# Kernel optimization log

Measured on AMD Instinct MI355X. Metric: run time of the kernel, lower is better.

The kernel has to match this reference:

```python
import jax, jax.numpy as jnp
import numpy as np

B, S, HID = 2, 2048, 2048
NH, NKV, HD = 32, 8, 64
ROPE_THETA = 10000.0
SCALE = HD ** -0.5


def _rope_cos_sin(seq_len, head_dim, theta):
    inv_freq = 1.0 / (theta ** (jnp.arange(0, head_dim, 2, dtype=jnp.float32) / head_dim))
    pos = jnp.arange(seq_len, dtype=jnp.float32)
    freqs = jnp.outer(pos, inv_freq)              # [S, HD/2]
    emb = jnp.concatenate([freqs, freqs], axis=-1)  # [S, HD]
    return jnp.cos(emb), jnp.sin(emb)


def _rotate_half(x):
    x1, x2 = jnp.split(x, 2, axis=-1)
    return jnp.concatenate([-x2, x1], axis=-1)


def setup_inputs() -> dict:
    key = jax.random.key(0)
    ks = jax.random.split(key, 8)
    s = 0.02
    return {
        "hidden_states": jax.random.normal(ks[0], (B, S, HID), jnp.float32),
        "q_w": jax.random.normal(ks[1], (NH * HD, HID), jnp.float32) * s,
        "q_b": jax.random.normal(ks[2], (NH * HD,), jnp.float32) * s,
        "k_w": jax.random.normal(ks[3], (NKV * HD, HID), jnp.float32) * s,
        "k_b": jax.random.normal(ks[4], (NKV * HD,), jnp.float32) * s,
        "v_w": jax.random.normal(ks[5], (NKV * HD, HID), jnp.float32) * s,
        "v_b": jax.random.normal(ks[6], (NKV * HD,), jnp.float32) * s,
        "o_w": jax.random.normal(ks[7], (HID, NH * HD), jnp.float32) * s,
    }


def reference(hidden_states, q_w, q_b, k_w, k_b, v_w, v_b, o_w):
    bsz, q_len, _ = hidden_states.shape
    # QKV projections (nn.Linear: x @ W^T + b)
    q = hidden_states @ q_w.T + q_b   # [B, S, NH*HD]
    k = hidden_states @ k_w.T + k_b   # [B, S, NKV*HD]
    v = hidden_states @ v_w.T + v_b
    # reshape to [B, H, S, D]
    q = q.reshape(bsz, q_len, NH, HD).transpose(0, 2, 1, 3)
    k = k.reshape(bsz, q_len, NKV, HD).transpose(0, 2, 1, 3)
    v = v.reshape(bsz, q_len, NKV, HD).transpose(0, 2, 1, 3)
    # RoPE
    cos, sin = _rope_cos_sin(q_len, HD, ROPE_THETA)  # [S, HD]
    cos = cos[None, None]; sin = sin[None, None]
    q = q * cos + _rotate_half(q) * sin
    k = k * cos + _rotate_half(k) * sin
    # GQA: expand kv heads to match query heads
    groups = NH // NKV
    k = jnp.repeat(k, groups, axis=1)  # [B, NH, S, D]
    v = jnp.repeat(v, groups, axis=1)
    # scaled dot-product attention with causal mask
    scores = jnp.einsum('bhqd,bhkd->bhqk', q, k) * SCALE
    causal = jnp.tril(jnp.ones((q_len, q_len), dtype=bool))
    scores = jnp.where(causal[None, None], scores, jnp.finfo(scores.dtype).min)
    probs = jax.nn.softmax(scores, axis=-1)
    out = jnp.einsum('bhqk,bhkd->bhqd', probs, v)  # [B, NH, S, D]
    out = out.transpose(0, 2, 1, 3).reshape(bsz, q_len, NH * HD)
    return out @ o_w.T  # [B, S, HID]
```

## Files before the change

kernel.cpp:

```cpp
#include <hip/hip_runtime.h>
#include <stdint.h>
#include <stddef.h>

typedef __attribute__((ext_vector_type(8))) short s16x8;
typedef __attribute__((ext_vector_type(4))) short s16x4;
typedef __attribute__((ext_vector_type(4))) float f32x4;
typedef __attribute__((ext_vector_type(2))) unsigned int u32x2;

#define S_LEN 2048
#define HID 2048
#define QKV_N 3072
#define NHEAD 32
#define NKVH 8

__device__ __forceinline__ unsigned short f2bf(float f) {
  union { float f; unsigned u; } a; a.f = f;
  unsigned u = a.u;
  u += 0x7fffu + ((u >> 16) & 1u);
  return (unsigned short)(u >> 16);
}
__device__ __forceinline__ unsigned cvt_pk_bf16(float a, float b) {
  unsigned r;
  asm("v_cvt_pk_bf16_f32 %0, %1, %2" : "=v"(r) : "v"(a), "v"(b));
  return r;
}
__device__ __forceinline__ void gl_lds16(const unsigned short* g, short* l) {
  __builtin_amdgcn_global_load_lds(
      (const __attribute__((address_space(1))) unsigned int*)g,
      (__attribute__((address_space(3))) unsigned int*)l, 16, 0, 0);
}

__global__ void k_convert(const float* __restrict__ x, const float* __restrict__ wq,
                          const float* __restrict__ wk, const float* __restrict__ wv,
                          const float* __restrict__ wo, unsigned short* __restrict__ dst) {
  const unsigned n4 = 18874368u / 4u;
  for (unsigned i = blockIdx.x * blockDim.x + threadIdx.x; i < n4;
       i += gridDim.x * blockDim.x) {
    unsigned e = i * 4u;
    const float* src; unsigned off;
    if (e < 8388608u)       { src = x;  off = e; }
    else if (e < 12582912u) { src = wq; off = e - 8388608u; }
    else if (e < 13631488u) { src = wk; off = e - 12582912u; }
    else if (e < 14680064u) { src = wv; off = e - 13631488u; }
    else                    { src = wo; off = e - 14680064u; }
    f32x4 v = *(const f32x4*)(src + off);
    s16x4 o;
    o[0] = (short)f2bf(v[0]); o[1] = (short)f2bf(v[1]);
    o[2] = (short)f2bf(v[2]); o[3] = (short)f2bf(v[3]);
    *(s16x4*)(dst + e) = o;
  }
}

__global__ void k_rope_table(float* __restrict__ cost, float* __restrict__ sint) {
  int idx = blockIdx.x * 256 + threadIdx.x;
  int i = idx & 31, s = idx >> 5;
  float inv = powf(10000.0f, -(float)(2 * i) / 64.0f);
  float ang = (float)s * inv;
  cost[idx] = cosf(ang);
  sint[idx] = sinf(ang);
}

template <int MODE>
__global__ __launch_bounds__(256) void k_gemm(
    const unsigned short* __restrict__ A,
    const unsigned short* __restrict__ W0, const unsigned short* __restrict__ W1,
    const unsigned short* __restrict__ W2,
    const float* __restrict__ b0, const float* __restrict__ b1, const float* __restrict__ b2,
    const float* __restrict__ ct, const float* __restrict__ st,
    unsigned short* __restrict__ Cb, float* __restrict__ Cf) {
  __shared__ short lA[3][4096];
  __shared__ short lB[3][4096];
  const int K = 2048;
  int tid = threadIdx.x;
  int wave = tid >> 6, lane = tid & 63;
  int l15 = lane & 15, lg = lane >> 4;
  int nwg = gridDim.x * gridDim.y;
  int f = blockIdx.y * gridDim.x + blockIdx.x;
  f = (f & 7) * (nwg >> 3) + (f >> 3);
  int tn = f % gridDim.x, tm = f / gridDim.x;

  const unsigned short* W; const float* bias = nullptr; int col0;
  if constexpr (MODE == 0) {
    if (tn < 16)      { W = W0; bias = b0; col0 = tn * 128; }
    else if (tn < 20) { W = W1; bias = b1; col0 = (tn - 16) * 128; }
    else              { W = W2; bias = b2; col0 = (tn - 20) * 128; }
  } else { W = W0; col0 = tn * 128; }
  int m0 = tm * 128;
  int wm = wave >> 1, wn = wave & 1;

  const unsigned short* gA0 = A + (size_t)(m0 + (tid >> 2)) * K + (tid & 3) * 8;
  const unsigned short* gA1 = gA0 + (size_t)64 * K;
  const unsigned short* gB0 = W + (size_t)(col0 + (tid >> 2)) * K + (tid & 3) * 8;
  const unsigned short* gB1 = gB0 + (size_t)64 * K;

  f32x4 acc[4][4];
#pragma unroll
  for (int m = 0; m < 4; ++m)
#pragma unroll
    for (int n = 0; n < 4; ++n) acc[m][n] = (f32x4){0.f, 0.f, 0.f, 0.f};

#pragma unroll
  for (int p = 0; p < 2; ++p) {
    int off = p * 32;
    gl_lds16(gA0 + off, &lA[p][wave * 512]);
    gl_lds16(gA1 + off, &lA[p][2048 + wave * 512]);
    gl_lds16(gB0 + off, &lB[p][wave * 512]);
    gl_lds16(gB1 + off, &lB[p][2048 + wave * 512]);
  }

  int cur = 0;
  for (int kt = 0; kt < 64; ++kt) {
    asm volatile("s_waitcnt vmcnt(4)" ::: "memory");
    __builtin_amdgcn_s_barrier();
    __builtin_amdgcn_sched_barrier(0);
    if (kt + 2 < 64) {
      int nx = cur + 2; if (nx >= 3) nx -= 3;
      int off = (kt + 2) * 32;
      gl_lds16(gA0 + off, &lA[nx][wave * 512]);
      gl_lds16(gA1 + off, &lA[nx][2048 + wave * 512]);
      gl_lds16(gB0 + off, &lB[nx][wave * 512]);
      gl_lds16(gB1 + off, &lB[nx][2048 + wave * 512]);
    }
    s16x8 af[4], bfr[4];
    const short* pa = &lA[cur][(wm * 64 + l15) * 32 + lg * 8];
    const short* pb = &lB[cur][(wn * 64 + l15) * 32 + lg * 8];
#pragma unroll
    for (int m = 0; m < 4; ++m) af[m] = *(const s16x8*)(pa + m * 512);
#pragma unroll
    for (int n = 0; n < 4; ++n) bfr[n] = *(const s16x8*)(pb + n * 512);
    __builtin_amdgcn_s_setprio(1);
#pragma unroll
    for (int m = 0; m < 4; ++m)
#pragma unroll
      for (int n = 0; n < 4; ++n)
        acc[m][n] = __builtin_amdgcn_mfma_f32_16x16x32_bf16(af[m], bfr[n], acc[m][n], 0, 0, 0);
    __builtin_amdgcn_s_setprio(0);
    cur = (cur + 1 == 3) ? 0 : cur + 1;
  }

  if constexpr (MODE == 0) {
    const float CSC = 0.125f * 1.44269504f;
    bool rope = (tn < 20);
    bool isq = (tn < 16);
#pragma unroll
    for (int n = 0; n < 2; ++n) {
      int lcol = col0 + wn * 64 + n * 16 + l15;
      int gcol = tn * 128 + wn * 64 + n * 16 + l15;
      float blo = bias[lcol], bhi = bias[lcol + 32];
      int i = n * 16 + l15;
#pragma unroll
      for (int m = 0; m < 4; ++m) {
        int row = m0 + wm * 64 + m * 16 + lg * 4;
#pragma unroll
        for (int r = 0; r < 4; ++r) {
          float xl = acc[m][n][r] + blo;
          float xh = acc[m][n + 2][r] + bhi;
          if (rope) {
            int s = (row + r) & (S_LEN - 1);
            float c = ct[s * 32 + i], sn = st[s * 32 + i];
            float nl = xl * c - xh * sn;
            xh = xh * c + xl * sn;
            xl = nl;
            if (isq) { xl *= CSC; xh *= CSC; }
          }
          Cb[(size_t)(row + r) * QKV_N + gcol] = f2bf(xl);
          Cb[(size_t)(row + r) * QKV_N + gcol + 32] = f2bf(xh);
        }
      }
    }
  } else {
#pragma unroll
    for (int n = 0; n < 4; ++n) {
      int gcol = tn * 128 + wn * 64 + n * 16 + l15;
#pragma unroll
      for (int m = 0; m < 4; ++m) {
        int row = m0 + wm * 64 + m * 16 + lg * 4;
#pragma unroll
        for (int r = 0; r < 4; ++r)
          Cf[(size_t)(row + r) * HID + gcol] = acc[m][n][r];
      }
    }
  }
}

__global__ void k_vtrans(const unsigned short* __restrict__ qkv, unsigned short* __restrict__ vt) {
  __shared__ unsigned short t[64][80];
  int ts = blockIdx.x & 63, td = blockIdx.x >> 6;
  int tid = threadIdx.x;
#pragma unroll
  for (int L = 0; L < 2; ++L) {
    int c = L * 256 + tid;
    int row = c >> 3, ch = c & 7;
    const unsigned short* src = qkv + (size_t)(ts * 64 + row) * QKV_N + 2560 + td * 64 + ch * 8;
    s16x8 v = *(const s16x8*)src;
    int cs = (ch * 8) ^ ((row >> 3) << 3);
    *(s16x8*)&t[row][cs] = v;
  }
  __syncthreads();
  int b = (ts * 64) >> 11;
  int s0 = (ts * 64) & (S_LEN - 1);
#pragma unroll
  for (int L = 0; L < 2; ++L) {
    int c = L * 256 + tid;
    int d = c >> 3, sc = c & 7;
    s16x8 o;
#pragma unroll
    for (int j = 0; j < 8; ++j) o[j] = (short)t[sc * 8 + j][d ^ (sc << 3)];
    unsigned short* dst = vt + ((size_t)((b * 8 + td) * 64 + d)) * 2048 + s0 + sc * 8;
    *(s16x8*)dst = o;
  }
}

__global__ __launch_bounds__(512, 4) void k_attn(const unsigned short* __restrict__ qkv,
                                                 const unsigned short* __restrict__ vt,
                                                 unsigned short* __restrict__ aout) {
  __shared__ unsigned short lK[2][4096];
  __shared__ unsigned short lV[2][4096];
  __shared__ unsigned short pl[8][1024];
  int wave = threadIdx.x >> 6, lane = threadIdx.x & 63;
  int l15 = lane & 15, lg = lane >> 4;
  int bi = blockIdx.x;
  int t  = 63 - (bi >> 4);
  int b  = (bi >> 3) & 1;
  int hg = bi & 7;
  int wh = wave >> 1;
  int mh = wave & 1;
  int h  = hg * 4 + wh;
  int q0 = t * 32 + mh * 16;
  int kbmax = t >> 1;

  const unsigned short* qb_ = qkv + (size_t)(b * S_LEN) * QKV_N + h * 64;
  const unsigned short* kbase = qkv + (size_t)(b * S_LEN) * QKV_N + 2048 + hg * 64;
  const unsigned short* vbase = vt + (size_t)((b * NKVH + hg) * 64) * 2048;
  unsigned short* pw = &pl[wave][0];
  int sw = (l15 & 7) << 3;

  int srow = wave * 8 + (lane >> 3);
  int ssw = 8 * ((lane & 7) ^ ((lane >> 3) & 7));
  const unsigned short* gk0 = kbase + (size_t)srow * QKV_N + ssw;
  const unsigned short* gv0 = vbase + (size_t)srow * 2048 + ssw;
  short* lkd0 = (short*)&lK[0][wave * 512]; short* lkd1 = (short*)&lK[1][wave * 512];
  short* lvd0 = (short*)&lV[0][wave * 512]; short* lvd1 = (short*)&lV[1][wave * 512];

  s16x8 aq[2];
#pragma unroll
  for (int ks = 0; ks < 2; ++ks)
    aq[ks] = *(const s16x8*)(qb_ + (size_t)(q0 + l15) * QKV_N + ks * 32 + lg * 8);

  f32x4 acc[4];
#pragma unroll
  for (int dt = 0; dt < 4; ++dt) acc[dt] = (f32x4){0.f, 0.f, 0.f, 0.f};
  float lrow = 0.f;

  gl_lds16(gk0, lkd0);
  gl_lds16(gv0, lvd0);
  asm volatile("s_waitcnt vmcnt(0)" ::: "memory");
  __syncthreads();

  for (int kb = 0; kb <= kbmax; ++kb) {
    const unsigned short* lk = &lK[kb & 1][0];
    const unsigned short* lv = &lV[kb & 1][0];
    if (kb < kbmax) {
      size_t go = (size_t)(kb + 1) * 64;
      if ((kb & 1) == 0) { gl_lds16(gk0 + go * QKV_N, lkd1); gl_lds16(gv0 + go, lvd1); }
      else               { gl_lds16(gk0 + go * QKV_N, lkd0); gl_lds16(gv0 + go, lvd0); }
    }
    bool need_mask = (kb == kbmax);
    f32x4 z[4];
    __builtin_amdgcn_s_setprio(1);
#pragma unroll
    for (int nt = 0; nt < 4; ++nt) {
      s16x8 k0 = *(const s16x8*)(lk + (nt * 16 + l15) * 64 + ((lg * 8) ^ sw));
      s16x8 k1 = *(const s16x8*)(lk + (nt * 16 + l15) * 64 + ((32 + lg * 8) ^ sw));
      f32x4 zz = (f32x4){0.f, 0.f, 0.f, 0.f};
      zz = __builtin_amdgcn_mfma_f32_16x16x32_bf16(k0, aq[0], zz, 0, 0, 0);
      zz = __builtin_amdgcn_mfma_f32_16x16x32_bf16(k1, aq[1], zz, 0, 0, 0);
      z[nt] = zz;
    }
    __builtin_amdgcn_s_setprio(0);
    int q = q0 + l15;
    float rs = 0.f;
#pragma unroll
    for (int nt = 0; nt < 4; ++nt) {
      float p[4];
#pragma unroll
      for (int r = 0; r < 4; ++r) {
        float v = z[nt][r];
        if (need_mask) {
          int k = kb * 64 + nt * 16 + lg * 4 + r;
          if (k > q) v = -1.0e30f;
        }
        p[r] = __builtin_amdgcn_exp2f(v);
      }
      rs += (p[0] + p[1]) + (p[2] + p[3]);
      u32x2 w;
      w[0] = cvt_pk_bf16(p[0], p[1]);
      w[1] = cvt_pk_bf16(p[2], p[3]);
      *(u32x2*)(pw + l15 * 64 + ((nt * 16 + lg * 4) ^ sw)) = w;
    }
    rs += __shfl_xor(rs, 16);
    rs += __shfl_xor(rs, 32);
    lrow += rs;
    s16x8 pa0 = *(const s16x8*)(pw + l15 * 64 + ((lg * 8) ^ sw));
    s16x8 pa1 = *(const s16x8*)(pw + l15 * 64 + ((32 + lg * 8) ^ sw));
    __builtin_amdgcn_s_setprio(1);
#pragma unroll
    for (int dt = 0; dt < 4; ++dt) {
      s16x8 v0 = *(const s16x8*)(lv + (dt * 16 + l15) * 64 + ((lg * 8) ^ sw));
      s16x8 v1 = *(const s16x8*)(lv + (dt * 16 + l15) * 64 + ((32 + lg * 8) ^ sw));
      acc[dt] = __builtin_amdgcn_mfma_f32_16x16x32_bf16(pa0, v0, acc[dt], 0, 0, 0);
      acc[dt] = __builtin_amdgcn_mfma_f32_16x16x32_bf16(pa1, v1, acc[dt], 0, 0, 0);
    }
    __builtin_amdgcn_s_setprio(0);
    asm volatile("s_waitcnt vmcnt(0)" ::: "memory");
    __syncthreads();
  }

  unsigned short* ob = aout + (size_t)(b * S_LEN) * HID + h * 64;
#pragma unroll
  for (int r = 0; r < 4; ++r) {
    float lr = __shfl(lrow, lg * 4 + r);
    float inv = 1.0f / lr;
#pragma unroll
    for (int dt = 0; dt < 4; ++dt)
      ob[(size_t)(q0 + lg * 4 + r) * HID + dt * 16 + l15] = f2bf(acc[dt][r] * inv);
  }
}

extern "C" void kernel_launch(void* const* d_in, const int* in_sizes, int n_in,
                              void* d_out, int out_size, void* d_ws, size_t ws_size,
                              hipStream_t stream) {
  const float* x  = (const float*)d_in[0];
  const float* qw = (const float*)d_in[1];
  const float* qb = (const float*)d_in[2];
  const float* kw = (const float*)d_in[3];
  const float* kbias = (const float*)d_in[4];
  const float* vw = (const float*)d_in[5];
  const float* vbias = (const float*)d_in[6];
  const float* ow = (const float*)d_in[7];

  unsigned short* Xb  = (unsigned short*)d_ws;
  unsigned short* Wqb = Xb + 8388608;
  unsigned short* Wkb = Wqb + 4194304;
  unsigned short* Wvb = Wkb + 1048576;
  unsigned short* Wob = Wvb + 1048576;
  unsigned short* QKV = Wob + 4194304;
  unsigned short* VT  = QKV + 12582912;
  unsigned short* AO  = VT + 2097152;
  float* COS = (float*)(AO + 8388608);
  float* SIN = COS + 65536;

  k_convert<<<1024, 256, 0, stream>>>(x, qw, kw, vw, ow, Xb);
  k_rope_table<<<256, 256, 0, stream>>>(COS, SIN);
  k_gemm<0><<<dim3(24, 32), 256, 0, stream>>>(Xb, Wqb, Wkb, Wvb, qb, kbias, vbias,
                                              COS, SIN, QKV, nullptr);
  k_vtrans<<<512, 256, 0, stream>>>(QKV, VT);
  k_attn<<<1024, 512, 0, stream>>>(QKV, VT, AO);
  k_gemm<1><<<dim3(16, 32), 256, 0, stream>>>(AO, Wob, nullptr, nullptr,
                                              nullptr, nullptr, nullptr, nullptr, nullptr,
                                              nullptr, (float*)d_out);
}
```

Measured before the change: 190.9 us.

## Use dedicated 256x128 tile kernel with 8 waves for output projection GEMM

Splits the templated GEMM into a QKV kernel and a separate output-projection kernel that uses 512-thread blocks computing 256x128 tiles, so each B tile loaded into LDS is shared by twice as many rows. The output GEMM grid drops from 512 to 256 blocks, which halves redundant weight loads but leaves fewer blocks to fill the GPU. It also makes the last pipeline iteration wait for all outstanding loads (vmcnt(0)) instead of vmcnt(4), which tightens correctness of the triple-buffered prefetch.

```diff
diff --git a/kernel.cpp b/kernel.cpp
--- a/kernel.cpp
+++ b/kernel.cpp
@@ -60,14 +60,13 @@
   sint[idx] = sinf(ang);
 }
 
-template <int MODE>
-__global__ __launch_bounds__(256) void k_gemm(
+__global__ __launch_bounds__(256) void k_gemm0(
     const unsigned short* __restrict__ A,
     const unsigned short* __restrict__ W0, const unsigned short* __restrict__ W1,
     const unsigned short* __restrict__ W2,
     const float* __restrict__ b0, const float* __restrict__ b1, const float* __restrict__ b2,
     const float* __restrict__ ct, const float* __restrict__ st,
-    unsigned short* __restrict__ Cb, float* __restrict__ Cf) {
+    unsigned short* __restrict__ Cb) {
   __shared__ short lA[3][4096];
   __shared__ short lB[3][4096];
   const int K = 2048;
@@ -79,12 +78,10 @@
   f = (f & 7) * (nwg >> 3) + (f >> 3);
   int tn = f % gridDim.x, tm = f / gridDim.x;
 
-  const unsigned short* W; const float* bias = nullptr; int col0;
-  if constexpr (MODE == 0) {
-    if (tn < 16)      { W = W0; bias = b0; col0 = tn * 128; }
-    else if (tn < 20) { W = W1; bias = b1; col0 = (tn - 16) * 128; }
-    else              { W = W2; bias = b2; col0 = (tn - 20) * 128; }
-  } else { W = W0; col0 = tn * 128; }
+  const unsigned short* W; const float* bias; int col0;
+  if (tn < 16)      { W = W0; bias = b0; col0 = tn * 128; }
+  else if (tn < 20) { W = W1; bias = b1; col0 = (tn - 16) * 128; }
+  else              { W = W2; bias = b2; col0 = (tn - 20) * 128; }
   int m0 = tm * 128;
   int wm = wave >> 1, wn = wave & 1;
 
@@ -110,7 +107,8 @@
 
   int cur = 0;
   for (int kt = 0; kt < 64; ++kt) {
-    asm volatile("s_waitcnt vmcnt(4)" ::: "memory");
+    if (kt < 63) asm volatile("s_waitcnt vmcnt(4)" ::: "memory");
+    else         asm volatile("s_waitcnt vmcnt(0)" ::: "memory");
     __builtin_amdgcn_s_barrier();
     __builtin_amdgcn_sched_barrier(0);
     if (kt + 2 < 64) {
@@ -138,47 +136,112 @@
     cur = (cur + 1 == 3) ? 0 : cur + 1;
   }
 
-  if constexpr (MODE == 0) {
-    const float CSC = 0.125f * 1.44269504f;
-    bool rope = (tn < 20);
-    bool isq = (tn < 16);
-#pragma unroll
-    for (int n = 0; n < 2; ++n) {
-      int lcol = col0 + wn * 64 + n * 16 + l15;
-      int gcol = tn * 128 + wn * 64 + n * 16 + l15;
-      float blo = bias[lcol], bhi = bias[lcol + 32];
-      int i = n * 16 + l15;
-#pragma unroll
-      for (int m = 0; m < 4; ++m) {
-        int row = m0 + wm * 64 + m * 16 + lg * 4;
-#pragma unroll
-        for (int r = 0; r < 4; ++r) {
-          float xl = acc[m][n][r] + blo;
-          float xh = acc[m][n + 2][r] + bhi;
-          if (rope) {
-            int s = (row + r) & (S_LEN - 1);
-            float c = ct[s * 32 + i], sn = st[s * 32 + i];
-            float nl = xl * c - xh * sn;
-            xh = xh * c + xl * sn;
-            xl = nl;
-            if (isq) { xl *= CSC; xh *= CSC; }
-          }
-          Cb[(size_t)(row + r) * QKV_N + gcol] = f2bf(xl);
-          Cb[(size_t)(row + r) * QKV_N + gcol + 32] = f2bf(xh);
+  const float CSC = 0.125f * 1.44269504f;
+  bool rope = (tn < 20);
+  bool isq = (tn < 16);
+#pragma unroll
+  for (int n = 0; n < 2; ++n) {
+    int lcol = col0 + wn * 64 + n * 16 + l15;
+    int gcol = tn * 128 + wn * 64 + n * 16 + l15;
+    float blo = bias[lcol], bhi = bias[lcol + 32];
+    int i = n * 16 + l15;
+#pragma unroll
+    for (int m = 0; m < 4; ++m) {
+      int row = m0 + wm * 64 + m * 16 + lg * 4;
+#pragma unroll
+      for (int r = 0; r < 4; ++r) {
+        float xl = acc[m][n][r] + blo;
+        float xh = acc[m][n + 2][r] + bhi;
+        if (rope) {
+          int s = (row + r) & (S_LEN - 1);
+          float c = ct[s * 32 + i], sn = st[s * 32 + i];
+          float nl = xl * c - xh * sn;
+          xh = xh * c + xl * sn;
+          xl = nl;
+          if (isq) { xl *= CSC; xh *= CSC; }
         }
+        Cb[(size_t)(row + r) * QKV_N + gcol] = f2bf(xl);
+        Cb[(size_t)(row + r) * QKV_N + gcol + 32] = f2bf(xh);
       }
     }
-  } else {
-#pragma unroll
-    for (int n = 0; n < 4; ++n) {
-      int gcol = tn * 128 + wn * 64 + n * 16 + l15;
-#pragma unroll
-      for (int m = 0; m < 4; ++m) {
-        int row = m0 + wm * 64 + m * 16 + lg * 4;
-#pragma unroll
-        for (int r = 0; r < 4; ++r)
-          Cf[(size_t)(row + r) * HID + gcol] = acc[m][n][r];
-      }
+  }
+}
+
+__global__ __launch_bounds__(512, 4) void k_gemm2(
+    const unsigned short* __restrict__ A,
+    const unsigned short* __restrict__ W,
+    float* __restrict__ Cf) {
+  __shared__ short lA[3][8192];
+  __shared__ short lB[3][4096];
+  const int K = 2048;
+  int tid = threadIdx.x;
+  int wave = tid >> 6, lane = tid & 63;
+  int l15 = lane & 15, lg = lane >> 4;
+  int f = blockIdx.x;
+  f = (f & 7) * 32 + (f >> 3);
+  int tn = f & 15, tm = f >> 4;
+  int m0 = tm * 256, col0 = tn * 128;
+  int wm = wave >> 1, wn = wave & 1;
+
+  int sr = lane >> 2;
+  int sc = (lane & 3) * 8;
+  const unsigned short* gA0 = A + (size_t)(m0 + wave * 32 + sr) * K + sc;
+  const unsigned short* gA1 = gA0 + (size_t)16 * K;
+  const unsigned short* gB0 = W + (size_t)(col0 + wave * 16 + sr) * K + sc;
+
+  f32x4 acc[4][4];
+#pragma unroll
+  for (int m = 0; m < 4; ++m)
+#pragma unroll
+    for (int n = 0; n < 4; ++n) acc[m][n] = (f32x4){0.f, 0.f, 0.f, 0.f};
+
+#pragma unroll
+  for (int p = 0; p < 2; ++p) {
+    int off = p * 32;
+    gl_lds16(gA0 + off, &lA[p][wave * 1024 + lane * 8]);
+    gl_lds16(gA1 + off, &lA[p][wave * 1024 + 512 + lane * 8]);
+    gl_lds16(gB0 + off, &lB[p][wave * 512 + lane * 8]);
+  }
+
+  int cur = 0;
+  for (int kt = 0; kt < 64; ++kt) {
+    if (kt < 63) asm volatile("s_waitcnt vmcnt(3)" ::: "memory");
+    else         asm volatile("s_waitcnt vmcnt(0)" ::: "memory");
+    __builtin_amdgcn_s_barrier();
+    __builtin_amdgcn_sched_barrier(0);
+    if (kt + 2 < 64) {
+      int nx = cur + 2; if (nx >= 3) nx -= 3;
+      int off = (kt + 2) * 32;
+      gl_lds16(gA0 + off, &lA[nx][wave * 1024 + lane * 8]);
+      gl_lds16(gA1 + off, &lA[nx][wave * 1024 + 512 + lane * 8]);
+      gl_lds16(gB0 + off, &lB[nx][wave * 512 + lane * 8]);
+    }
+    s16x8 af[4], bfr[4];
+    const short* pa = &lA[cur][(wm * 64 + l15) * 32 + lg * 8];
+    const short* pb = &lB[cur][(wn * 64 + l15) * 32 + lg * 8];
+#pragma unroll
+    for (int m = 0; m < 4; ++m) af[m] = *(const s16x8*)(pa + m * 512);
+#pragma unroll
+    for (int n = 0; n < 4; ++n) bfr[n] = *(const s16x8*)(pb + n * 512);
+    __builtin_amdgcn_s_setprio(1);
+#pragma unroll
+    for (int m = 0; m < 4; ++m)
+#pragma unroll
+      for (int n = 0; n < 4; ++n)
+        acc[m][n] = __builtin_amdgcn_mfma_f32_16x16x32_bf16(af[m], bfr[n], acc[m][n], 0, 0, 0);
+    __builtin_amdgcn_s_setprio(0);
+    cur = (cur + 1 == 3) ? 0 : cur + 1;
+  }
+
+#pragma unroll
+  for (int n = 0; n < 4; ++n) {
+    int gcol = col0 + wn * 64 + n * 16 + l15;
+#pragma unroll
+    for (int m = 0; m < 4; ++m) {
+      int row = m0 + wm * 64 + m * 16 + lg * 4;
+#pragma unroll
+      for (int r = 0; r < 4; ++r)
+        Cf[(size_t)(row + r) * HID + gcol] = acc[m][n][r];
     }
   }
 }
@@ -352,11 +415,9 @@
 
   k_convert<<<1024, 256, 0, stream>>>(x, qw, kw, vw, ow, Xb);
   k_rope_table<<<256, 256, 0, stream>>>(COS, SIN);
-  k_gemm<0><<<dim3(24, 32), 256, 0, stream>>>(Xb, Wqb, Wkb, Wvb, qb, kbias, vbias,
-                                              COS, SIN, QKV, nullptr);
+  k_gemm0<<<dim3(24, 32), 256, 0, stream>>>(Xb, Wqb, Wkb, Wvb, qb, kbias, vbias,
+                                            COS, SIN, QKV);
   k_vtrans<<<512, 256, 0, stream>>>(QKV, VT);
   k_attn<<<1024, 512, 0, stream>>>(QKV, VT, AO);
-  k_gemm<1><<<dim3(16, 32), 256, 0, stream>>>(AO, Wob, nullptr, nullptr,
-                                              nullptr, nullptr, nullptr, nullptr, nullptr,
-                                              nullptr, (float*)d_out);
-}
+  k_gemm2<<<256, 512, 0, stream>>>(AO, Wob, (float*)d_out);
+}
```

After: 195.8 us. 2.6% more time.

## Use 256x256 eight-wave GEMM tiles with swizzled LDS and interleaved staging

Applied to the files above, without the earlier changes.

Replaces the 128x128, four-wave GEMM with a 256x256, eight-wave kernel that steps K by 64 and double-buffers XOR-swizzled LDS tiles. Global loads for the next K step are staged in quarters between the MFMA phases. The aim is more operand reuse per loaded byte, fewer LDS bank conflicts, and load latency hidden behind compute. The cost is far fewer workgroups (192 and 128), which may leave many CUs idle, plus a large LDS footprint that limits occupancy.

```diff
diff --git a/kernel.cpp b/kernel.cpp
--- a/kernel.cpp
+++ b/kernel.cpp
@@ -61,124 +61,168 @@
 }
 
 template <int MODE>
-__global__ __launch_bounds__(256) void k_gemm(
+__global__ __launch_bounds__(512, 2) void k_gemm8(
     const unsigned short* __restrict__ A,
     const unsigned short* __restrict__ W0, const unsigned short* __restrict__ W1,
     const unsigned short* __restrict__ W2,
     const float* __restrict__ b0, const float* __restrict__ b1, const float* __restrict__ b2,
     const float* __restrict__ ct, const float* __restrict__ st,
-    unsigned short* __restrict__ Cb, float* __restrict__ Cf) {
-  __shared__ short lA[3][4096];
-  __shared__ short lB[3][4096];
-  const int K = 2048;
+    unsigned short* __restrict__ Cb, float* __restrict__ Cf, int ntn) {
+  __shared__ short sA[2][16384];
+  __shared__ short sB[2][16384];
+  const int K = 2048, NT = 32;
   int tid = threadIdx.x;
-  int wave = tid >> 6, lane = tid & 63;
+  int w = tid >> 6, lane = tid & 63;
   int l15 = lane & 15, lg = lane >> 4;
-  int nwg = gridDim.x * gridDim.y;
-  int f = blockIdx.y * gridDim.x + blockIdx.x;
+  int wm = w >> 2, wn = w & 3;
+  int nwg = gridDim.x;
+  int f = blockIdx.x;
   f = (f & 7) * (nwg >> 3) + (f >> 3);
-  int tn = f % gridDim.x, tm = f / gridDim.x;
-
-  const unsigned short* W; const float* bias = nullptr; int col0;
+  int tn = f % ntn, tm = f / ntn;
+
+  const unsigned short* W; const float* bias = nullptr; int bcol0;
   if constexpr (MODE == 0) {
-    if (tn < 16)      { W = W0; bias = b0; col0 = tn * 128; }
-    else if (tn < 20) { W = W1; bias = b1; col0 = (tn - 16) * 128; }
-    else              { W = W2; bias = b2; col0 = (tn - 20) * 128; }
-  } else { W = W0; col0 = tn * 128; }
-  int m0 = tm * 128;
-  int wm = wave >> 1, wn = wave & 1;
-
-  const unsigned short* gA0 = A + (size_t)(m0 + (tid >> 2)) * K + (tid & 3) * 8;
-  const unsigned short* gA1 = gA0 + (size_t)64 * K;
-  const unsigned short* gB0 = W + (size_t)(col0 + (tid >> 2)) * K + (tid & 3) * 8;
-  const unsigned short* gB1 = gB0 + (size_t)64 * K;
-
-  f32x4 acc[4][4];
+    if (tn < 8)       { W = W0; bias = b0; bcol0 = tn * 256; }
+    else if (tn < 10) { W = W1; bias = b1; bcol0 = (tn - 8) * 256; }
+    else              { W = W2; bias = b2; bcol0 = (tn - 10) * 256; }
+  } else { W = W0; bcol0 = tn * 256; }
+  int m0 = tm * 256;
+
+  int sr8 = lane >> 3;
+  int scol = ((lane & 7) ^ sr8) * 8;
+
+  auto stageA = [&](int p, int mh, int t) {
+#pragma unroll
+    for (int j = 0; j < 2; ++j) {
+      int lrow0 = j * 128 + mh * 64 + w * 8;
+      gl_lds16(A + (size_t)(m0 + lrow0 + sr8) * K + t * 64 + scol,
+               &sA[p][lrow0 * 64] + lane * 8);
+    }
+  };
+  auto stageB = [&](int p, int hb, int t) {
+#pragma unroll
+    for (int j = 0; j < 2; ++j) {
+      int lrow0 = hb * 128 + j * 64 + w * 8;
+      gl_lds16(W + (size_t)(bcol0 + lrow0 + sr8) * K + t * 64 + scol,
+               &sB[p][lrow0 * 64] + lane * 8);
+    }
+  };
+  auto ldA = [&](s16x8* d, int p, int mh, int ks) {
+#pragma unroll
+    for (int fm = 0; fm < 4; ++fm) {
+      int row = wm * 128 + mh * 64 + fm * 16 + l15;
+      d[fm] = *(const s16x8*)&sA[p][row * 64 + (((ks * 4 + lg) ^ (row & 7)) << 3)];
+    }
+  };
+  auto ldB = [&](s16x8* d, int p, int ks) {
+#pragma unroll
+    for (int fn = 0; fn < 4; ++fn) {
+      int row = wn * 64 + fn * 16 + l15;
+      d[fn] = *(const s16x8*)&sB[p][row * 64 + (((ks * 4 + lg) ^ (row & 7)) << 3)];
+    }
+  };
+
+  f32x4 accL[4][4], accH[4][4];
 #pragma unroll
   for (int m = 0; m < 4; ++m)
 #pragma unroll
-    for (int n = 0; n < 4; ++n) acc[m][n] = (f32x4){0.f, 0.f, 0.f, 0.f};
-
-#pragma unroll
-  for (int p = 0; p < 2; ++p) {
-    int off = p * 32;
-    gl_lds16(gA0 + off, &lA[p][wave * 512]);
-    gl_lds16(gA1 + off, &lA[p][2048 + wave * 512]);
-    gl_lds16(gB0 + off, &lB[p][wave * 512]);
-    gl_lds16(gB1 + off, &lB[p][2048 + wave * 512]);
-  }
-
-  int cur = 0;
-  for (int kt = 0; kt < 64; ++kt) {
-    asm volatile("s_waitcnt vmcnt(4)" ::: "memory");
+    for (int n = 0; n < 4; ++n) {
+      accL[m][n] = (f32x4){0.f, 0.f, 0.f, 0.f};
+      accH[m][n] = (f32x4){0.f, 0.f, 0.f, 0.f};
+    }
+
+  auto MM = [&](s16x8 (&a)[4], s16x8 (&bb)[4], f32x4 (&ac)[4][4]) {
+    __builtin_amdgcn_s_setprio(1);
+#pragma unroll
+    for (int fm = 0; fm < 4; ++fm)
+#pragma unroll
+      for (int fn = 0; fn < 4; ++fn)
+        ac[fm][fn] = __builtin_amdgcn_mfma_f32_16x16x32_bf16(a[fm], bb[fn], ac[fm][fn], 0, 0, 0);
+    __builtin_amdgcn_s_setprio(0);
+  };
+
+  stageA(0, 0, 0); stageB(0, 0, 0); stageB(0, 1, 0); stageA(0, 1, 0);
+  asm volatile("s_waitcnt vmcnt(2)" ::: "memory");
+  __builtin_amdgcn_s_barrier();
+
+  for (int t = 0; t < NT; ++t) {
+    int p = t & 1, pn = p ^ 1;
+    bool stg = (t + 1 < NT);
+    s16x8 a[4], Bk0[4], Bk1[4];
+    ldB(Bk0, p, 0); ldA(a, p, 0, 0);
+    if (stg) stageA(pn, 0, t + 1);
+    __builtin_amdgcn_s_barrier();
+    MM(a, Bk0, accL);
+    __builtin_amdgcn_s_barrier();
+    ldB(Bk1, p, 1); ldA(a, p, 0, 1);
+    if (stg) stageB(pn, 0, t + 1);
+    __builtin_amdgcn_s_barrier();
+    MM(a, Bk1, accL);
+    if (t == NT - 1) asm volatile("s_waitcnt vmcnt(0)" ::: "memory");
+    else             asm volatile("s_waitcnt vmcnt(4)" ::: "memory");
     __builtin_amdgcn_s_barrier();
     __builtin_amdgcn_sched_barrier(0);
-    if (kt + 2 < 64) {
-      int nx = cur + 2; if (nx >= 3) nx -= 3;
-      int off = (kt + 2) * 32;
-      gl_lds16(gA0 + off, &lA[nx][wave * 512]);
-      gl_lds16(gA1 + off, &lA[nx][2048 + wave * 512]);
-      gl_lds16(gB0 + off, &lB[nx][wave * 512]);
-      gl_lds16(gB1 + off, &lB[nx][2048 + wave * 512]);
-    }
-    s16x8 af[4], bfr[4];
-    const short* pa = &lA[cur][(wm * 64 + l15) * 32 + lg * 8];
-    const short* pb = &lB[cur][(wn * 64 + l15) * 32 + lg * 8];
-#pragma unroll
-    for (int m = 0; m < 4; ++m) af[m] = *(const s16x8*)(pa + m * 512);
-#pragma unroll
-    for (int n = 0; n < 4; ++n) bfr[n] = *(const s16x8*)(pb + n * 512);
-    __builtin_amdgcn_s_setprio(1);
-#pragma unroll
-    for (int m = 0; m < 4; ++m)
-#pragma unroll
-      for (int n = 0; n < 4; ++n)
-        acc[m][n] = __builtin_amdgcn_mfma_f32_16x16x32_bf16(af[m], bfr[n], acc[m][n], 0, 0, 0);
-    __builtin_amdgcn_s_setprio(0);
-    cur = (cur + 1 == 3) ? 0 : cur + 1;
+    ldA(a, p, 1, 0);
+    if (stg) stageB(pn, 1, t + 1);
+    __builtin_amdgcn_s_barrier();
+    MM(a, Bk0, accH);
+    __builtin_amdgcn_s_barrier();
+    ldA(a, p, 1, 1);
+    if (stg) stageA(pn, 1, t + 1);
+    __builtin_amdgcn_s_barrier();
+    MM(a, Bk1, accH);
+    asm volatile("s_waitcnt vmcnt(2)" ::: "memory");
+    __builtin_amdgcn_s_barrier();
+    __builtin_amdgcn_sched_barrier(0);
   }
 
   if constexpr (MODE == 0) {
     const float CSC = 0.125f * 1.44269504f;
-    bool rope = (tn < 20);
-    bool isq = (tn < 16);
-#pragma unroll
-    for (int n = 0; n < 2; ++n) {
-      int lcol = col0 + wn * 64 + n * 16 + l15;
-      int gcol = tn * 128 + wn * 64 + n * 16 + l15;
+    bool rope = (tn < 10), isq = (tn < 8);
+#pragma unroll
+    for (int fn = 0; fn < 2; ++fn) {
+      int lcol = bcol0 + wn * 64 + fn * 16 + l15;
+      int gcol = tn * 256 + wn * 64 + fn * 16 + l15;
       float blo = bias[lcol], bhi = bias[lcol + 32];
-      int i = n * 16 + l15;
-#pragma unroll
-      for (int m = 0; m < 4; ++m) {
-        int row = m0 + wm * 64 + m * 16 + lg * 4;
-#pragma unroll
-        for (int r = 0; r < 4; ++r) {
-          float xl = acc[m][n][r] + blo;
-          float xh = acc[m][n + 2][r] + bhi;
-          if (rope) {
-            int s = (row + r) & (S_LEN - 1);
-            float c = ct[s * 32 + i], sn = st[s * 32 + i];
-            float nl = xl * c - xh * sn;
-            xh = xh * c + xl * sn;
-            xl = nl;
-            if (isq) { xl *= CSC; xh *= CSC; }
+      int i = fn * 16 + l15;
+#pragma unroll
+      for (int mh = 0; mh < 2; ++mh)
+#pragma unroll
+        for (int fm = 0; fm < 4; ++fm) {
+          int row = m0 + wm * 128 + mh * 64 + fm * 16 + lg * 4;
+          f32x4 vlo = mh ? accH[fm][fn] : accL[fm][fn];
+          f32x4 vhi = mh ? accH[fm][fn + 2] : accL[fm][fn + 2];
+#pragma unroll
+          for (int r = 0; r < 4; ++r) {
+            float xl = vlo[r] + blo;
+            float xh = vhi[r] + bhi;
+            if (rope) {
+              int s = (row + r) & (S_LEN - 1);
+              float c = ct[s * 32 + i], sn = st[s * 32 + i];
+              float nl = xl * c - xh * sn;
+              xh = xh * c + xl * sn;
+              xl = nl;
+              if (isq) { xl *= CSC; xh *= CSC; }
+            }
+            Cb[(size_t)(row + r) * QKV_N + gcol] = f2bf(xl);
+            Cb[(size_t)(row + r) * QKV_N + gcol + 32] = f2bf(xh);
           }
-          Cb[(size_t)(row + r) * QKV_N + gcol] = f2bf(xl);
-          Cb[(size_t)(row + r) * QKV_N + gcol + 32] = f2bf(xh);
         }
-      }
     }
   } else {
 #pragma unroll
-    for (int n = 0; n < 4; ++n) {
-      int gcol = tn * 128 + wn * 64 + n * 16 + l15;
-#pragma unroll
-      for (int m = 0; m < 4; ++m) {
-        int row = m0 + wm * 64 + m * 16 + lg * 4;
-#pragma unroll
-        for (int r = 0; r < 4; ++r)
-          Cf[(size_t)(row + r) * HID + gcol] = acc[m][n][r];
-      }
+    for (int fn = 0; fn < 4; ++fn) {
+      int gcol = tn * 256 + wn * 64 + fn * 16 + l15;
+#pragma unroll
+      for (int mh = 0; mh < 2; ++mh)
+#pragma unroll
+        for (int fm = 0; fm < 4; ++fm) {
+          int row = m0 + wm * 128 + mh * 64 + fm * 16 + lg * 4;
+          f32x4 v = mh ? accH[fm][fn] : accL[fm][fn];
+#pragma unroll
+          for (int r = 0; r < 4; ++r)
+            Cf[(size_t)(row + r) * HID + gcol] = v[r];
+        }
     }
   }
 }
@@ -352,11 +396,11 @@
 
   k_convert<<<1024, 256, 0, stream>>>(x, qw, kw, vw, ow, Xb);
   k_rope_table<<<256, 256, 0, stream>>>(COS, SIN);
-  k_gemm<0><<<dim3(24, 32), 256, 0, stream>>>(Xb, Wqb, Wkb, Wvb, qb, kbias, vbias,
-                                              COS, SIN, QKV, nullptr);
+  k_gemm8<0><<<192, 512, 0, stream>>>(Xb, Wqb, Wkb, Wvb, qb, kbias, vbias,
+                                      COS, SIN, QKV, nullptr, 12);
   k_vtrans<<<512, 256, 0, stream>>>(QKV, VT);
   k_attn<<<1024, 512, 0, stream>>>(QKV, VT, AO);
-  k_gemm<1><<<dim3(16, 32), 256, 0, stream>>>(AO, Wob, nullptr, nullptr,
-                                              nullptr, nullptr, nullptr, nullptr, nullptr,
-                                              nullptr, (float*)d_out);
-}
+  k_gemm8<1><<<128, 512, 0, stream>>>(AO, Wob, nullptr, nullptr,
+                                      nullptr, nullptr, nullptr, nullptr, nullptr,
+                                      nullptr, (float*)d_out, 8);
+}
```

Result: slower. 213.3 us (+11.8%).
